# Kernel tuning notes

Hardware: AMD Instinct MI355X
Metric: run time of the kernel (lower is better)

The kernel has to match this reference:

```python
import jax, jax.numpy as jnp
import numpy as np

N, C, NUM_GROUPS = 4_194_304, 16, 8


def setup_inputs() -> dict:
    key = jax.random.key(0)
    k1, k2, k3 = jax.random.split(key, 3)
    input_ = jax.random.normal(k1, (N, C), dtype=jnp.float32)
    target = jax.random.randint(k2, (N,), 0, C, dtype=jnp.int64) if jax.config.jax_enable_x64 else jax.random.randint(k2, (N,), 0, C, dtype=jnp.int32)
    group = jax.random.randint(k3, (N,), 0, NUM_GROUPS, dtype=jnp.int32)
    return {"input_": input_, "target": target, "group": group}


def reference(input_, target, group):
    # gather input_[i, target[i]] and take |1 - .|
    err = jnp.abs(1.0 - jnp.take_along_axis(input_, target[:, None].astype(jnp.int32), axis=1)[:, 0])  # [N]
    # per-group mean == L1-row-normalized one-hot matmul in the original
    sums = jax.ops.segment_sum(err, group, num_segments=NUM_GROUPS)               # [G]
    counts = jax.ops.segment_sum(jnp.ones_like(err), group, num_segments=NUM_GROUPS)
    means = jnp.where(counts > 0, sums / jnp.maximum(counts, 1.0), 0.0)           # empty group -> 0 (F.normalize eps behavior)
    loss_target_value = 0.5
    return jnp.abs(loss_target_value - means.mean())
```

## Files before the change

### kernel.cpp

```cpp
#include <hip/hip_runtime.h>

#define N_ELEMS 4194304
#define C_DIM 16
#define G_NUM 8


__global__ __launch_bounds__(256) void berl_partial(
    const float* __restrict__ input_,
    const int*   __restrict__ target,
    const int*   __restrict__ group,
    float*        __restrict__ g_sums,
    unsigned int* __restrict__ g_counts)
{
    __shared__ float        s_sums[G_NUM];
    __shared__ unsigned int s_counts[G_NUM];
    const int tid = threadIdx.x;
    if (tid < G_NUM) { s_sums[tid] = 0.0f; s_counts[tid] = 0u; }
    __syncthreads();

    float sums[G_NUM];
    float cnts[G_NUM];
#pragma unroll
    for (int g = 0; g < G_NUM; ++g) { sums[g] = 0.0f; cnts[g] = 0.0f; }

    const int4* t4 = (const int4*)target;
    const int4* g4 = (const int4*)group;
    const int n4     = N_ELEMS / 4;
    const int stride = gridDim.x * blockDim.x;

    for (int i = blockIdx.x * blockDim.x + tid; i < n4; i += stride) {
        int4 t = t4[i];
        int4 g = g4[i];
        const int base = i * (4 * C_DIM);
        float e0 = fabsf(1.0f - __builtin_nontemporal_load(&input_[base + 0 * C_DIM + t.x]));
        float e1 = fabsf(1.0f - __builtin_nontemporal_load(&input_[base + 1 * C_DIM + t.y]));
        float e2 = fabsf(1.0f - __builtin_nontemporal_load(&input_[base + 2 * C_DIM + t.z]));
        float e3 = fabsf(1.0f - __builtin_nontemporal_load(&input_[base + 3 * C_DIM + t.w]));
#pragma unroll
        for (int k = 0; k < G_NUM; ++k) {
            sums[k] += (g.x == k) ? e0 : 0.0f;
            sums[k] += (g.y == k) ? e1 : 0.0f;
            sums[k] += (g.z == k) ? e2 : 0.0f;
            sums[k] += (g.w == k) ? e3 : 0.0f;
            cnts[k] += (g.x == k) ? 1.0f : 0.0f;
            cnts[k] += (g.y == k) ? 1.0f : 0.0f;
            cnts[k] += (g.z == k) ? 1.0f : 0.0f;
            cnts[k] += (g.w == k) ? 1.0f : 0.0f;
        }
    }

#pragma unroll
    for (int k = 0; k < G_NUM; ++k) {
        atomicAdd(&s_sums[k], sums[k]);
        atomicAdd(&s_counts[k], (unsigned int)cnts[k]);
    }
    __syncthreads();

    if (tid < G_NUM) {
        atomicAdd(&g_sums[tid], s_sums[tid]);
        atomicAdd(&g_counts[tid], s_counts[tid]);
    }
}

__global__ void berl_final(const float* __restrict__ g_sums,
                           const unsigned int* __restrict__ g_counts,
                           float* __restrict__ out)
{
    if (threadIdx.x == 0 && blockIdx.x == 0) {
        float acc = 0.0f;
#pragma unroll
        for (int g = 0; g < G_NUM; ++g) {
            float c = (float)g_counts[g];
            float m = (c > 0.0f) ? (g_sums[g] / fmaxf(c, 1.0f)) : 0.0f;
            acc += m;
        }
        out[0] = fabsf(0.5f - acc / (float)G_NUM);
    }
}

extern "C" void kernel_launch(void* const* d_in, const int* in_sizes, int n_in,
                              void* d_out, int out_size, void* d_ws, size_t ws_size,
                              hipStream_t stream) {
    const float* input_ = (const float*)d_in[0];
    const int*   target = (const int*)d_in[1];
    const int*   group  = (const int*)d_in[2];
    float* out = (float*)d_out;

    float*        g_sums   = (float*)d_ws;
    unsigned int* g_counts = (unsigned int*)((char*)d_ws + G_NUM * sizeof(float));

    hipMemsetAsync(d_ws, 0, G_NUM * (sizeof(float) + sizeof(unsigned int)), stream);

    dim3 block(256);
    dim3 grid(2048);
    berl_partial<<<grid, block, 0, stream>>>(input_, target, group, g_sums, g_counts);
    berl_final<<<1, 64, 0, stream>>>(g_sums, g_counts, out);
}
```

Baseline: 415.3 us.

## Read full rows with 4-lane cliques and drop global atomics and memset

Each row is now handled by a clique of four lanes. Every lane loads one 16-byte vector of the row, so the input is streamed coalesced and in full rather than as scattered 4-byte gathers. Each lane picks the target element with selects when it owns that quarter of the row. Per-block partial sums are written to a workspace buffer and reduced by a second kernel, which replaces the global atomics and the memset launch. The change reads the whole 256 MB input instead of touching only sectors, and it loads target and group four times redundantly per row.

```diff
diff --git a/kernel.cpp b/kernel.cpp
--- a/kernel.cpp
+++ b/kernel.cpp
@@ -4,77 +4,103 @@
 #define C_DIM 16
 #define G_NUM 8
 
+#define BLOCKS 2048
+#define TPB 256
+#define NTHREADS (BLOCKS * TPB)
+#define NCLIQUES (NTHREADS / 4)
+#define ITERS (N_ELEMS / NCLIQUES)
 
-__global__ __launch_bounds__(256) void berl_partial(
+typedef float vfloat4 __attribute__((ext_vector_type(4)));
+
+
+__global__ __launch_bounds__(TPB) void berl_partial(
     const float* __restrict__ input_,
     const int*   __restrict__ target,
     const int*   __restrict__ group,
-    float*        __restrict__ g_sums,
-    unsigned int* __restrict__ g_counts)
+    float*       __restrict__ part)
 {
-    __shared__ float        s_sums[G_NUM];
-    __shared__ unsigned int s_counts[G_NUM];
-    const int tid = threadIdx.x;
-    if (tid < G_NUM) { s_sums[tid] = 0.0f; s_counts[tid] = 0u; }
-    __syncthreads();
+    const int tid   = threadIdx.x;
+    const int lane  = tid & 3;
+    const int gcliq = (blockIdx.x * TPB + tid) >> 2;
 
     float sums[G_NUM];
     float cnts[G_NUM];
 #pragma unroll
-    for (int g = 0; g < G_NUM; ++g) { sums[g] = 0.0f; cnts[g] = 0.0f; }
+    for (int k = 0; k < G_NUM; ++k) { sums[k] = 0.0f; cnts[k] = 0.0f; }
 
-    const int4* t4 = (const int4*)target;
-    const int4* g4 = (const int4*)group;
-    const int n4     = N_ELEMS / 4;
-    const int stride = gridDim.x * blockDim.x;
+    const vfloat4* in4 = (const vfloat4*)input_;
 
-    for (int i = blockIdx.x * blockDim.x + tid; i < n4; i += stride) {
-        int4 t = t4[i];
-        int4 g = g4[i];
-        const int base = i * (4 * C_DIM);
-        float e0 = fabsf(1.0f - __builtin_nontemporal_load(&input_[base + 0 * C_DIM + t.x]));
-        float e1 = fabsf(1.0f - __builtin_nontemporal_load(&input_[base + 1 * C_DIM + t.y]));
-        float e2 = fabsf(1.0f - __builtin_nontemporal_load(&input_[base + 2 * C_DIM + t.z]));
-        float e3 = fabsf(1.0f - __builtin_nontemporal_load(&input_[base + 3 * C_DIM + t.w]));
+#pragma unroll 4
+    for (int it = 0; it < ITERS; ++it) {
+        const int row = gcliq + it * NCLIQUES;
+        vfloat4 v = __builtin_nontemporal_load(&in4[row * 4 + lane]);
+        const int t = target[row];
+        const int g = group[row];
+
+        const int e2 = t & 3;
+        float x = v.x;
+        x = (e2 == 1) ? v.y : x;
+        x = (e2 == 2) ? v.z : x;
+        x = (e2 == 3) ? v.w : x;
+
+        const bool own = ((t >> 2) == lane);
+        const float e  = own ? fabsf(1.0f - x) : 0.0f;
+        const float c1 = own ? 1.0f : 0.0f;
+
 #pragma unroll
         for (int k = 0; k < G_NUM; ++k) {
-            sums[k] += (g.x == k) ? e0 : 0.0f;
-            sums[k] += (g.y == k) ? e1 : 0.0f;
-            sums[k] += (g.z == k) ? e2 : 0.0f;
-            sums[k] += (g.w == k) ? e3 : 0.0f;
-            cnts[k] += (g.x == k) ? 1.0f : 0.0f;
-            cnts[k] += (g.y == k) ? 1.0f : 0.0f;
-            cnts[k] += (g.z == k) ? 1.0f : 0.0f;
-            cnts[k] += (g.w == k) ? 1.0f : 0.0f;
+            sums[k] += (g == k) ? e  : 0.0f;
+            cnts[k] += (g == k) ? c1 : 0.0f;
         }
     }
 
+    __shared__ float s_sums[G_NUM];
+    __shared__ float s_cnts[G_NUM];
+    if (tid < G_NUM) { s_sums[tid] = 0.0f; s_cnts[tid] = 0.0f; }
+    __syncthreads();
 #pragma unroll
     for (int k = 0; k < G_NUM; ++k) {
         atomicAdd(&s_sums[k], sums[k]);
-        atomicAdd(&s_counts[k], (unsigned int)cnts[k]);
+        atomicAdd(&s_cnts[k], cnts[k]);
+    }
+    __syncthreads();
+    if (tid < G_NUM)            part[blockIdx.x * 16 + tid] = s_sums[tid];
+    else if (tid < 2 * G_NUM)   part[blockIdx.x * 16 + tid] = s_cnts[tid - G_NUM];
+}
+
+__global__ __launch_bounds__(256) void berl_final(
+    const float* __restrict__ part,
+    float*       __restrict__ out)
+{
+    __shared__ float s_acc[256];
+    __shared__ float s_tot[16];
+    const int tid = threadIdx.x;
+    const int j   = tid & 15;
+    const int b0  = tid >> 4;
+
+    float acc = 0.0f;
+    for (int k = 0; k < BLOCKS / 16; ++k)
+        acc += part[(b0 + 16 * k) * 16 + j];
+    s_acc[tid] = acc;
+    __syncthreads();
+
+    if (tid < 16) {
+        float tot = 0.0f;
+#pragma unroll
+        for (int r = 0; r < 16; ++r) tot += s_acc[r * 16 + tid];
+        s_tot[tid] = tot;
     }
     __syncthreads();
 
-    if (tid < G_NUM) {
-        atomicAdd(&g_sums[tid], s_sums[tid]);
-        atomicAdd(&g_counts[tid], s_counts[tid]);
-    }
-}
-
-__global__ void berl_final(const float* __restrict__ g_sums,
-                           const unsigned int* __restrict__ g_counts,
-                           float* __restrict__ out)
-{
-    if (threadIdx.x == 0 && blockIdx.x == 0) {
-        float acc = 0.0f;
+    if (tid == 0) {
+        float acc2 = 0.0f;
 #pragma unroll
         for (int g = 0; g < G_NUM; ++g) {
-            float c = (float)g_counts[g];
-            float m = (c > 0.0f) ? (g_sums[g] / fmaxf(c, 1.0f)) : 0.0f;
-            acc += m;
+            const float c = s_tot[8 + g];
+            const float m = (c > 0.0f) ? (s_tot[g] / fmaxf(c, 1.0f)) : 0.0f;
+            acc2 += m;
         }
-        out[0] = fabsf(0.5f - acc / (float)G_NUM);
+        out[0] = fabsf(0.5f - acc2 / (float)G_NUM);
     }
 }
 
@@ -84,15 +110,11 @@
     const float* input_ = (const float*)d_in[0];
     const int*   target = (const int*)d_in[1];
     const int*   group  = (const int*)d_in[2];
-    float* out = (float*)d_out;
+    float* out  = (float*)d_out;
+    float* part = (float*)d_ws;
 
-    float*        g_sums   = (float*)d_ws;
-    unsigned int* g_counts = (unsigned int*)((char*)d_ws + G_NUM * sizeof(float));
-
-    hipMemsetAsync(d_ws, 0, G_NUM * (sizeof(float) + sizeof(unsigned int)), stream);
-
-    dim3 block(256);
-    dim3 grid(2048);
-    berl_partial<<<grid, block, 0, stream>>>(input_, target, group, g_sums, g_counts);
-    berl_final<<<1, 64, 0, stream>>>(g_sums, g_counts, out);
+    dim3 block(TPB);
+    dim3 grid(BLOCKS);
+    berl_partial<<<grid, block, 0, stream>>>(input_, target, group, part);
+    berl_final<<<1, 256, 0, stream>>>(part, out);
 }
```

Result: slower. 427.7 us (+3.0%).
